# Optimization experiments

Measured on AMD Instinct MI355X. Metric: run time of the kernel, lower is better.

Reference implementation:

```python
import jax, jax.numpy as jnp
import numpy as np

N, F, H, K, T, O = 4096, 64, 64, 2, 5, 32  # nodes, in_feat, hidden, heads, temporal_steps, out


def setup_inputs() -> dict:
    key = jax.random.key(0)
    ks = jax.random.split(key, 12)
    s = 0.05
    return {
        "node_features": jax.random.normal(ks[0], (N, F), jnp.float32),
        "adj_matrix": jax.random.randint(ks[1], (N, N), 0, 2, jnp.int32),
        "temporal_features": jax.random.normal(ks[2], (N, T, H), jnp.float32),
        # GAT params (stacked over K heads). Linear W: Wh = h @ W.T, so W_gat[k] is [H, F].
        "W_gat": jax.random.normal(ks[3], (K, H, F), jnp.float32) * s,
        "a_src": jax.random.normal(ks[4], (K, H), jnp.float32) * s,  # first half of a (repeat -> column/neighbor index)
        "a_dst": jax.random.normal(ks[5], (K, H), jnp.float32) * s,  # second half of a (repeat_interleave -> row/self index)
        # LSTM (1 layer, input K*H, hidden H), PyTorch gate order i,f,g,o
        "W_ih": jax.random.normal(ks[6], (4 * H, K * H), jnp.float32) * s,
        "W_hh": jax.random.normal(ks[7], (4 * H, H), jnp.float32) * s,
        "b_ih": jax.random.normal(ks[8], (4 * H,), jnp.float32) * s,
        "b_hh": jax.random.normal(ks[9], (4 * H,), jnp.float32) * s,
        # fc
        "fc_W": jax.random.normal(ks[10], (O, H), jnp.float32) * s,
        "fc_b": jax.random.normal(ks[11], (O,), jnp.float32) * s,
    }


def reference(node_features, adj_matrix, temporal_features,
              W_gat, a_src, a_dst, W_ih, W_hh, b_ih, b_hh, fc_W, fc_b):
    # ---- GAT heads (vectorized over K) ----
    Wh = jnp.einsum("nf,khf->knh", node_features, W_gat)          # [K,N,H]
    # a([Wh_i, Wh_j]) == a_src.Wh_j + a_dst.Wh_i; e[p,q] = lrelu(dst[p] + src[q])
    s_src = jnp.einsum("knh,kh->kn", Wh, a_src)                    # column term
    s_dst = jnp.einsum("knh,kh->kn", Wh, a_dst)                    # row term
    e = jax.nn.leaky_relu(s_dst[:, :, None] + s_src[:, None, :], 0.2)  # [K,N,N]
    e = jnp.where(adj_matrix[None, :, :] > 0, e, jnp.float32(-1e9))
    att = jax.nn.softmax(e, axis=-1)                               # dropout = identity (eval)
    h_prime = jax.nn.elu(jnp.einsum("kpq,kqh->kph", att, Wh))      # [K,N,H]
    h = jnp.transpose(h_prime, (1, 0, 2)).reshape(N, K * H)        # concat heads [N, K*H]
    # ---- LSTM over seq of length 1 (h.unsqueeze(1)); h0 = c0 = 0 ----
    gates = h @ W_ih.T + b_ih + b_hh                               # h0 @ W_hh.T == 0
    i, f, g, o = jnp.split(gates, 4, axis=-1)
    c = jax.nn.sigmoid(i) * jnp.tanh(g)                            # f * c0 == 0
    h_t = jax.nn.sigmoid(o) * jnp.tanh(c)                          # [N,H]
    return h_t @ fc_W.T + fc_b                                     # [N,O]
```

## Files before the change

### kernel.cpp

```cpp
#include <hip/hip_runtime.h>


#define NN 4096

typedef __attribute__((ext_vector_type(8))) short bf16x8;
typedef __attribute__((ext_vector_type(4))) float f32x4;

__device__ inline unsigned short bf_rne(float f) {
    unsigned u = __float_as_uint(f);
    u += 0x7fffu + ((u >> 16) & 1u);
    return (unsigned short)(u >> 16);
}

__device__ inline unsigned cvt_pk_bf16(float lo, float hi) {
    unsigned r;
    asm("v_cvt_pk_bf16_f32 %0, %1, %2" : "=v"(r) : "v"(lo), "v"(hi));
    return r;
}

__device__ inline float sigf(float x) { return 1.f / (1.f + __expf(-x)); }

__device__ inline unsigned pack16(const int4 a, const int4 b,
                                  const int4 c, const int4 d) {
    unsigned m = 0;
    m |= (a.x > 0) ? 0x0001u : 0u; m |= (a.y > 0) ? 0x0002u : 0u;
    m |= (a.z > 0) ? 0x0004u : 0u; m |= (a.w > 0) ? 0x0008u : 0u;
    m |= (b.x > 0) ? 0x0010u : 0u; m |= (b.y > 0) ? 0x0020u : 0u;
    m |= (b.z > 0) ? 0x0040u : 0u; m |= (b.w > 0) ? 0x0080u : 0u;
    m |= (c.x > 0) ? 0x0100u : 0u; m |= (c.y > 0) ? 0x0200u : 0u;
    m |= (c.z > 0) ? 0x0400u : 0u; m |= (c.w > 0) ? 0x0800u : 0u;
    m |= (d.x > 0) ? 0x1000u : 0u; m |= (d.y > 0) ? 0x2000u : 0u;
    m |= (d.z > 0) ? 0x4000u : 0u; m |= (d.w > 0) ? 0x8000u : 0u;
    return m;
}

__global__ __launch_bounds__(256) void prep_small(
    const float* __restrict__ X, const float* __restrict__ Wg,
    const float* __restrict__ a_src, const float* __restrict__ a_dst,
    const float* __restrict__ W_ih, const float* __restrict__ b_ih,
    const float* __restrict__ b_hh, const float* __restrict__ fc_W,
    unsigned short* __restrict__ whB, float* __restrict__ e1s,
    float* __restrict__ e2s, float* __restrict__ e1d, float* __restrict__ e2d,
    unsigned short* __restrict__ Wpk, unsigned short* __restrict__ fcb,
    float* __restrict__ biasg)
{
    __shared__ float X_lds[64][64];
    __shared__ float Wh_lds[64][65];
    __shared__ float spart[64][4][2];
    const int t = threadIdx.x;
    const int bid = blockIdx.x;

    if (bid >= 64) {
        const int idx = (bid - 64) * 256 + t;
        if (idx < 24576) {
            const int j = idx & 7, lane = (idx >> 3) & 63;
            const int k0 = (idx >> 9) & 3, tt = idx >> 11;
            const int jj = tt * 16 + (lane & 15);
            const int m = k0 * 32 + (lane >> 4) * 8 + j;
            const int sr = (jj < 64) ? jj : 64 + jj;
            Wpk[idx] = bf_rne(W_ih[sr * 128 + m]);
        } else if (idx < 26624) {
            const int o = idx - 24576;
            const int j = o & 7, lane = (o >> 3) & 63;
            const int k0 = (o >> 9) & 1, tt = o >> 10;
            const int row = tt * 16 + (lane & 15);
            const int m = k0 * 32 + (lane >> 4) * 8 + j;
            fcb[o] = bf_rne(fc_W[row * 64 + m]);
        } else if (idx < 26816) {
            const int j = idx - 26624;
            const int sr = (j < 64) ? j : 64 + j;
            biasg[j] = b_ih[sr] + b_hh[sr];
        }
        return;
    }

    const int n0 = bid * 64;
#pragma unroll
    for (int i = 0; i < 16; ++i) {
        int idx = t + i * 256;
        X_lds[idx >> 6][idx & 63] = X[n0 * 64 + idx];
    }
    __syncthreads();
    const int h = t & 63, rg = t >> 6;
    for (int k = 0; k < 2; ++k) {
        float acc[16];
#pragma unroll
        for (int r = 0; r < 16; ++r) acc[r] = 0.f;
        for (int f0 = 0; f0 < 64; f0 += 4) {
            const float4 w4 = *(const float4*)&Wg[(k * 64 + h) * 64 + f0];
#pragma unroll
            for (int r = 0; r < 16; ++r) {
                const float4 x4 = *(const float4*)&X_lds[rg * 16 + r][f0];
                acc[r] += w4.x * x4.x + w4.y * x4.y + w4.z * x4.z + w4.w * x4.w;
            }
        }
        if (k) __syncthreads();
#pragma unroll
        for (int r = 0; r < 16; ++r) Wh_lds[rg * 16 + r][h] = acc[r];
        __syncthreads();
        {
            const int r = t & 63, qa = t >> 6;
            float ps = 0.f, pd = 0.f;
#pragma unroll
            for (int i = 0; i < 16; ++i) {
                const int hh = qa * 16 + i;
                const float v = Wh_lds[r][hh];
                ps += v * a_src[k * 64 + hh];
                pd += v * a_dst[k * 64 + hh];
            }
            spart[r][qa][0] = ps;
            spart[r][qa][1] = pd;
        }
        {
#pragma unroll
            for (int pid = t; pid < 512; pid += 256) {
                const int n = pid & 15, qg = (pid >> 4) & 3;
                const int qb_loc = (pid >> 6) & 1, f = pid >> 7;
                const int qb = (n0 >> 5) + qb_loc;
                unsigned pk[4];
#pragma unroll
                for (int i = 0; i < 4; ++i) {
                    const int r = qb_loc * 32 + qg * 8 + 2 * i;
                    unsigned lo = bf_rne(Wh_lds[r][f * 16 + n]);
                    unsigned hi = bf_rne(Wh_lds[r + 1][f * 16 + n]);
                    pk[i] = lo | (hi << 16);
                }
                uint4* dst = (uint4*)&whB[(((k * 4 + f) * 128 + qb) * 512) + (qg * 16 + n) * 8];
                *dst = make_uint4(pk[0], pk[1], pk[2], pk[3]);
            }
        }
        __syncthreads();
        if (t < 64) {
            float s0 = spart[t][0][0] + spart[t][1][0] + spart[t][2][0] + spart[t][3][0];
            float s1 = spart[t][0][1] + spart[t][1][1] + spart[t][2][1] + spart[t][3][1];
            e1s[k * NN + n0 + t] = __expf(s0);
            e2s[k * NN + n0 + t] = __expf(0.2f * s0);
            e1d[k * NN + n0 + t] = __expf(s1);
            e2d[k * NN + n0 + t] = __expf(0.2f * s1);
        }
    }
}

__global__ __launch_bounds__(1024) void gat_attn(
    const int* __restrict__ adj,
    const unsigned short* __restrict__ whB,
    const float* __restrict__ e1s, const float* __restrict__ e2s,
    const float* __restrict__ e1d, const float* __restrict__ e2d,
    const unsigned short* __restrict__ Wpk, const unsigned short* __restrict__ fcb,
    const float* __restrict__ biasg, const float* __restrict__ fc_b,
    float* __restrict__ out)
{
    __shared__ float S_all[16][2][16][64];
    __shared__ float z_all[16][2][16];
    __shared__ unsigned short msk_lds[2][16][66];
    unsigned short* h_lds = (unsigned short*)&S_all[0][0][0][0];
    float* gate_lds = (float*)((char*)&S_all[0][0][0][0] + 4608);

    const int tid = threadIdx.x;
    const int wave = tid >> 6, lane = tid & 63;
    const int rloc = lane & 15, qg = lane >> 4;
    const int p0 = blockIdx.x * 16;
    const int p = p0 + rloc;

    const int4* __restrict__ arow = (const int4*)(adj + (long)(p0 + wave) * NN);

    const float e1p0 = e1d[p], e2p0 = e2d[p];
    const float e1p1 = e1d[NN + p], e2p1 = e2d[NN + p];
    const unsigned short* __restrict__ whB_l = whB + lane * 8;

    f32x4 acc[2][4];
#pragma unroll
    for (int k = 0; k < 2; ++k)
#pragma unroll
        for (int f = 0; f < 4; ++f)
            acc[k][f] = (f32x4){0.f, 0.f, 0.f, 0.f};
    float z0 = 0.f, z1 = 0.f;

    {
        const int4 a0 = arow[lane * 4 + 0];
        const int4 a1 = arow[lane * 4 + 1];
        const int4 a2 = arow[lane * 4 + 2];
        const int4 a3 = arow[lane * 4 + 3];
        msk_lds[0][wave][lane] = (unsigned short)pack16(a0, a1, a2, a3);
    }
    __syncthreads();

#pragma unroll
    for (int c = 0; c < 4; ++c) {
        int4 n0v, n1v, n2v, n3v;
        if (c < 3) {
            const int base = (c + 1) * 256 + lane * 4;
            n0v = arow[base + 0];
            n1v = arow[base + 1];
            n2v = arow[base + 2];
            n3v = arow[base + 3];
        }
#pragma unroll
        for (int kk = 0; kk < 2; ++kk) {
            const int q0 = c * 1024 + wave * 64 + kk * 32 + qg * 8;
            const int qb = c * 32 + wave * 2 + kk;
            const unsigned mm = msk_lds[c & 1][rloc][wave * 4 + kk * 2 + (qg >> 1)];
            const unsigned byte8 = (mm >> ((qg & 1) * 8)) & 0xffu;
            const float4 qa0 = *(const float4*)(e1s + q0);
            const float4 qa1 = *(const float4*)(e1s + q0 + 4);
            const float4 qb0 = *(const float4*)(e2s + q0);
            const float4 qb1 = *(const float4*)(e2s + q0 + 4);
            const float4 qc0 = *(const float4*)(e1s + NN + q0);
            const float4 qc1 = *(const float4*)(e1s + NN + q0 + 4);
            const float4 qd0 = *(const float4*)(e2s + NN + q0);
            const float4 qd1 = *(const float4*)(e2s + NN + q0 + 4);
            const float q1v0[8] = {qa0.x, qa0.y, qa0.z, qa0.w, qa1.x, qa1.y, qa1.z, qa1.w};
            const float q2v0[8] = {qb0.x, qb0.y, qb0.z, qb0.w, qb1.x, qb1.y, qb1.z, qb1.w};
            const float q1v1[8] = {qc0.x, qc0.y, qc0.z, qc0.w, qc1.x, qc1.y, qc1.z, qc1.w};
            const float q2v1[8] = {qd0.x, qd0.y, qd0.z, qd0.w, qd1.x, qd1.y, qd1.z, qd1.w};
            float w0a[8], w1a[8];
#pragma unroll
            for (int j = 0; j < 8; ++j) {
                const bool on = (byte8 & (1u << j)) != 0u;
                const float pp0 = e1p0 * q1v0[j];
                float w0 = pp0 > 1.f ? pp0 : e2p0 * q2v0[j];
                w0 = on ? w0 : 0.f;
                z0 += w0;
                w0a[j] = w0;
                const float pp1 = e1p1 * q1v1[j];
                float w1 = pp1 > 1.f ? pp1 : e2p1 * q2v1[j];
                w1 = on ? w1 : 0.f;
                z1 += w1;
                w1a[j] = w1;
            }
            union { bf16x8 v; unsigned w[4]; } fa0, fa1;
#pragma unroll
            for (int i = 0; i < 4; ++i) {
                fa0.w[i] = cvt_pk_bf16(w0a[2 * i], w0a[2 * i + 1]);
                fa1.w[i] = cvt_pk_bf16(w1a[2 * i], w1a[2 * i + 1]);
            }
#pragma unroll
            for (int f = 0; f < 4; ++f) {
                const bf16x8 b0 = *(const bf16x8*)(whB_l + ((f * 128 + qb) << 9));
                acc[0][f] = __builtin_amdgcn_mfma_f32_16x16x32_bf16(fa0.v, b0, acc[0][f], 0, 0, 0);
                const bf16x8 b1 = *(const bf16x8*)(whB_l + (((4 + f) * 128 + qb) << 9));
                acc[1][f] = __builtin_amdgcn_mfma_f32_16x16x32_bf16(fa1.v, b1, acc[1][f], 0, 0, 0);
            }
        }
        if (c < 3) {
            msk_lds[(c + 1) & 1][wave][lane] =
                (unsigned short)pack16(n0v, n1v, n2v, n3v);
            __syncthreads();
        }
    }
    z0 += __shfl_xor(z0, 16); z0 += __shfl_xor(z0, 32);
    z1 += __shfl_xor(z1, 16); z1 += __shfl_xor(z1, 32);
    if (lane < 16) { z_all[wave][0][lane] = z0; z_all[wave][1][lane] = z1; }
#pragma unroll
    for (int k = 0; k < 2; ++k)
#pragma unroll
        for (int f = 0; f < 4; ++f)
#pragma unroll
            for (int j = 0; j < 4; ++j)
                S_all[wave][k][qg * 4 + j][f * 16 + rloc] = acc[k][f][j];
    __syncthreads();
    float vreg[2]; int vk[2], vr[2], vh[2];
#pragma unroll
    for (int i = 0; i < 2; ++i) {
        const int idx = tid + i * 1024;
        const int k = idx >> 10, rr = (idx >> 6) & 15, hh = idx & 63;
        float s = 0.f, z = 0.f;
#pragma unroll
        for (int w = 0; w < 16; ++w) {
            s += S_all[w][k][rr][hh];
            z += z_all[w][k][rr];
        }
        float v = s / z;
        vreg[i] = v > 0.f ? v : expm1f(v);
        vk[i] = k; vr[i] = rr; vh[i] = hh;
    }
    __syncthreads();
#pragma unroll
    for (int i = 0; i < 2; ++i)
        h_lds[vr[i] * 136 + vk[i] * 64 + vh[i]] = bf_rne(vreg[i]);
    __syncthreads();

    const int c2 = lane & 15, g4 = lane >> 4;
    if (wave < 12) {
        const int t = wave;
        f32x4 ga = (f32x4){0.f, 0.f, 0.f, 0.f};
#pragma unroll
        for (int k0 = 0; k0 < 4; ++k0) {
            const bf16x8 a = *(const bf16x8*)&h_lds[c2 * 136 + k0 * 32 + g4 * 8];
            const bf16x8 b = *(const bf16x8*)&Wpk[((t * 4 + k0) * 64 + lane) * 8];
            ga = __builtin_amdgcn_mfma_f32_16x16x32_bf16(a, b, ga, 0, 0, 0);
        }
        const float bb = biasg[t * 16 + c2];
#pragma unroll
        for (int j = 0; j < 4; ++j)
            gate_lds[(t >> 2) * 1088 + (g4 * 4 + j) * 68 + (t & 3) * 16 + c2] = ga[j] + bb;
    }
    __syncthreads();
    {
        const int n = tid >> 6, hh = tid & 63;
        const float iv = gate_lds[n * 68 + hh];
        const float gv = gate_lds[1088 + n * 68 + hh];
        const float ov = gate_lds[2176 + n * 68 + hh];
        const float cv = sigf(iv) * tanhf(gv);
        const float htv = sigf(ov) * tanhf(cv);
        __syncthreads();
        h_lds[n * 136 + hh] = bf_rne(htv);
    }
    __syncthreads();
    if (wave < 2) {
        const int t2 = wave;
        f32x4 fa = (f32x4){0.f, 0.f, 0.f, 0.f};
#pragma unroll
        for (int k0 = 0; k0 < 2; ++k0) {
            const bf16x8 a = *(const bf16x8*)&h_lds[c2 * 136 + k0 * 32 + g4 * 8];
            const bf16x8 b = *(const bf16x8*)&fcb[((t2 * 2 + k0) * 64 + lane) * 8];
            fa = __builtin_amdgcn_mfma_f32_16x16x32_bf16(a, b, fa, 0, 0, 0);
        }
        const float fb = fc_b[t2 * 16 + c2];
#pragma unroll
        for (int j = 0; j < 4; ++j)
            out[(p0 + g4 * 4 + j) * 32 + t2 * 16 + c2] = fa[j] + fb;
    }
}

extern "C" void kernel_launch(void* const* d_in, const int* in_sizes, int n_in,
                              void* d_out, int out_size, void* d_ws, size_t ws_size,
                              hipStream_t stream) {
    const float* X     = (const float*)d_in[0];
    const int*   adj   = (const int*)d_in[1];
    const float* Wg    = (const float*)d_in[3];
    const float* a_src = (const float*)d_in[4];
    const float* a_dst = (const float*)d_in[5];
    const float* W_ih  = (const float*)d_in[6];
    const float* b_ih  = (const float*)d_in[8];
    const float* b_hh  = (const float*)d_in[9];
    const float* fc_W  = (const float*)d_in[10];
    const float* fc_b  = (const float*)d_in[11];
    float* out = (float*)d_out;

    char* ws = (char*)d_ws;
    unsigned short* whB = (unsigned short*)ws;
    float* e1s = (float*)(ws + (1 << 20));
    float* e2s = (float*)(ws + (1 << 20) + (32 << 10));
    float* e1d = (float*)(ws + (1 << 20) + (64 << 10));
    float* e2d = (float*)(ws + (1 << 20) + (96 << 10));
    char* ws2 = ws + (1 << 20) + (128 << 10);
    unsigned short* Wpk = (unsigned short*)ws2;
    unsigned short* fcb = (unsigned short*)(ws2 + (48 << 10));
    float* biasg = (float*)(ws2 + (52 << 10));

    hipLaunchKernelGGL(prep_small, dim3(169), dim3(256), 0, stream,
                       X, Wg, a_src, a_dst, W_ih, b_ih, b_hh, fc_W,
                       whB, e1s, e2s, e1d, e2d, Wpk, fcb, biasg);
    hipLaunchKernelGGL(gat_attn, dim3(256), dim3(1024), 0, stream,
                       adj, whB, e1s, e2s, e1d, e2d, Wpk, fcb, biasg, fc_b, out);
}
```

Measured before the change: 58.38 us.

## Coalesce adjacency row loads and prefetch mask two chunks ahead

Adjacency rows were read with each lane loading four consecutive int4s. Now each load instruction has consecutive lanes reading consecutive int4s (stride 64 across the four loads), which coalesces the global reads. The nibble packing of the 0/1 mask and the bit extraction from shared memory are remapped to fit this interleaved layout. The prefetch depth grows from one chunk to two, with register double buffering. This hides more of the global load latency at the cost of extra registers and more complex bit shuffling.

```diff
diff --git a/kernel.cpp b/kernel.cpp
--- a/kernel.cpp
+++ b/kernel.cpp
@@ -20,17 +20,12 @@
 
 __device__ inline float sigf(float x) { return 1.f / (1.f + __expf(-x)); }
 
-__device__ inline unsigned pack16(const int4 a, const int4 b,
-                                  const int4 c, const int4 d) {
+__device__ inline unsigned nib4(const int4 a) {
     unsigned m = 0;
-    m |= (a.x > 0) ? 0x0001u : 0u; m |= (a.y > 0) ? 0x0002u : 0u;
-    m |= (a.z > 0) ? 0x0004u : 0u; m |= (a.w > 0) ? 0x0008u : 0u;
-    m |= (b.x > 0) ? 0x0010u : 0u; m |= (b.y > 0) ? 0x0020u : 0u;
-    m |= (b.z > 0) ? 0x0040u : 0u; m |= (b.w > 0) ? 0x0080u : 0u;
-    m |= (c.x > 0) ? 0x0100u : 0u; m |= (c.y > 0) ? 0x0200u : 0u;
-    m |= (c.z > 0) ? 0x0400u : 0u; m |= (c.w > 0) ? 0x0800u : 0u;
-    m |= (d.x > 0) ? 0x1000u : 0u; m |= (d.y > 0) ? 0x2000u : 0u;
-    m |= (d.z > 0) ? 0x4000u : 0u; m |= (d.w > 0) ? 0x8000u : 0u;
+    m |= (a.x > 0) ? 1u : 0u;
+    m |= (a.y > 0) ? 2u : 0u;
+    m |= (a.z > 0) ? 4u : 0u;
+    m |= (a.w > 0) ? 8u : 0u;
     return m;
 }
 
@@ -152,7 +147,7 @@
 {
     __shared__ float S_all[16][2][16][64];
     __shared__ float z_all[16][2][16];
-    __shared__ unsigned short msk_lds[2][16][66];
+    __shared__ unsigned msk32[2][16][37];
     unsigned short* h_lds = (unsigned short*)&S_all[0][0][0][0];
     float* gate_lds = (float*)((char*)&S_all[0][0][0][0] + 4608);
 
@@ -162,7 +157,7 @@
     const int p0 = blockIdx.x * 16;
     const int p = p0 + rloc;
 
-    const int4* __restrict__ arow = (const int4*)(adj + (long)(p0 + wave) * NN);
+    const int4* __restrict__ arow4 = (const int4*)(adj + (long)(p0 + wave) * NN);
 
     const float e1p0 = e1d[p], e2p0 = e2d[p];
     const float e1p1 = e1d[NN + p], e2p1 = e2d[NN + p];
@@ -176,31 +171,33 @@
             acc[k][f] = (f32x4){0.f, 0.f, 0.f, 0.f};
     float z0 = 0.f, z1 = 0.f;
 
+    int4 pre[2][4];
+#pragma unroll
+    for (int o = 0; o < 4; ++o) pre[0][o] = arow4[o * 64 + lane];
+#pragma unroll
+    for (int o = 0; o < 4; ++o) pre[1][o] = arow4[256 + o * 64 + lane];
     {
-        const int4 a0 = arow[lane * 4 + 0];
-        const int4 a1 = arow[lane * 4 + 1];
-        const int4 a2 = arow[lane * 4 + 2];
-        const int4 a3 = arow[lane * 4 + 3];
-        msk_lds[0][wave][lane] = (unsigned short)pack16(a0, a1, a2, a3);
+        const unsigned pk = nib4(pre[0][0]) | (nib4(pre[0][1]) << 4) |
+                            (nib4(pre[0][2]) << 8) | (nib4(pre[0][3]) << 12);
+        ((unsigned short*)&msk32[0][wave][0])[lane] = (unsigned short)pk;
     }
     __syncthreads();
 
 #pragma unroll
     for (int c = 0; c < 4; ++c) {
-        int4 n0v, n1v, n2v, n3v;
-        if (c < 3) {
-            const int base = (c + 1) * 256 + lane * 4;
-            n0v = arow[base + 0];
-            n1v = arow[base + 1];
-            n2v = arow[base + 2];
-            n3v = arow[base + 3];
+        if (c + 2 < 4) {
+#pragma unroll
+            for (int o = 0; o < 4; ++o)
+                pre[c & 1][o] = arow4[(c + 2) * 256 + o * 64 + lane];
         }
 #pragma unroll
         for (int kk = 0; kk < 2; ++kk) {
             const int q0 = c * 1024 + wave * 64 + kk * 32 + qg * 8;
             const int qb = c * 32 + wave * 2 + kk;
-            const unsigned mm = msk_lds[c & 1][rloc][wave * 4 + kk * 2 + (qg >> 1)];
-            const unsigned byte8 = (mm >> ((qg & 1) * 8)) & 0xffu;
+            const unsigned W = msk32[c & 1][rloc][(wave & 3) * 8 + kk * 4 + qg];
+            const unsigned osel = (wave >> 2) * 4;
+            const unsigned byte8 = ((W >> osel) & 0xFu) |
+                                   (((W >> (16 + osel)) & 0xFu) << 4);
             const float4 qa0 = *(const float4*)(e1s + q0);
             const float4 qa1 = *(const float4*)(e1s + q0 + 4);
             const float4 qb0 = *(const float4*)(e2s + q0);
@@ -243,8 +240,9 @@
             }
         }
         if (c < 3) {
-            msk_lds[(c + 1) & 1][wave][lane] =
-                (unsigned short)pack16(n0v, n1v, n2v, n3v);
+            const unsigned pk = nib4(pre[(c + 1) & 1][0]) | (nib4(pre[(c + 1) & 1][1]) << 4) |
+                                (nib4(pre[(c + 1) & 1][2]) << 8) | (nib4(pre[(c + 1) & 1][3]) << 12);
+            ((unsigned short*)&msk32[(c + 1) & 1][wave][0])[lane] = (unsigned short)pk;
             __syncthreads();
         }
     }
```

Result: slower. 60.09 us (+2.9%).

## Split prep kernel into 16-node blocks and use nontemporal loads for adjacency

Applied to the files above, without the earlier changes.

The prep kernel now handles 16 nodes per block instead of 64, giving 256 compute blocks instead of 64 so more CUs are busy. It also computes both heads in one pass and writes the bf16-packed Wh in smaller 32-bit stores. The attention kernel reads the adjacency matrix with nontemporal loads to avoid polluting the cache with streamed data. The trade-off is more redundant reads of the weights per block and narrower stores.

```diff
diff --git a/kernel.cpp b/kernel.cpp
--- a/kernel.cpp
+++ b/kernel.cpp
@@ -5,6 +5,7 @@
 
 typedef __attribute__((ext_vector_type(8))) short bf16x8;
 typedef __attribute__((ext_vector_type(4))) float f32x4;
+typedef __attribute__((ext_vector_type(4))) int i32x4;
 
 __device__ inline unsigned short bf_rne(float f) {
     unsigned u = __float_as_uint(f);
@@ -20,8 +21,8 @@
 
 __device__ inline float sigf(float x) { return 1.f / (1.f + __expf(-x)); }
 
-__device__ inline unsigned pack16(const int4 a, const int4 b,
-                                  const int4 c, const int4 d) {
+__device__ inline unsigned pack16(const i32x4 a, const i32x4 b,
+                                  const i32x4 c, const i32x4 d) {
     unsigned m = 0;
     m |= (a.x > 0) ? 0x0001u : 0u; m |= (a.y > 0) ? 0x0002u : 0u;
     m |= (a.z > 0) ? 0x0004u : 0u; m |= (a.w > 0) ? 0x0008u : 0u;
@@ -34,7 +35,7 @@
     return m;
 }
 
-__global__ __launch_bounds__(256) void prep_small(
+__global__ __launch_bounds__(256) void prep_parallel(
     const float* __restrict__ X, const float* __restrict__ Wg,
     const float* __restrict__ a_src, const float* __restrict__ a_dst,
     const float* __restrict__ W_ih, const float* __restrict__ b_ih,
@@ -44,14 +45,14 @@
     unsigned short* __restrict__ Wpk, unsigned short* __restrict__ fcb,
     float* __restrict__ biasg)
 {
-    __shared__ float X_lds[64][64];
-    __shared__ float Wh_lds[64][65];
-    __shared__ float spart[64][4][2];
+    __shared__ float X_lds[16][64];
+    __shared__ float Wh_lds[2][16][68];
+    __shared__ float spart[32][8][2];
     const int t = threadIdx.x;
     const int bid = blockIdx.x;
 
-    if (bid >= 64) {
-        const int idx = (bid - 64) * 256 + t;
+    if (bid >= 256) {
+        const int idx = (bid - 256) * 256 + t;
         if (idx < 24576) {
             const int j = idx & 7, lane = (idx >> 3) & 63;
             const int k0 = (idx >> 9) & 3, tt = idx >> 11;
@@ -74,70 +75,75 @@
         return;
     }
 
-    const int n0 = bid * 64;
-#pragma unroll
-    for (int i = 0; i < 16; ++i) {
-        int idx = t + i * 256;
-        X_lds[idx >> 6][idx & 63] = X[n0 * 64 + idx];
-    }
-    __syncthreads();
-    const int h = t & 63, rg = t >> 6;
-    for (int k = 0; k < 2; ++k) {
-        float acc[16];
-#pragma unroll
-        for (int r = 0; r < 16; ++r) acc[r] = 0.f;
-        for (int f0 = 0; f0 < 64; f0 += 4) {
-            const float4 w4 = *(const float4*)&Wg[(k * 64 + h) * 64 + f0];
-#pragma unroll
-            for (int r = 0; r < 16; ++r) {
-                const float4 x4 = *(const float4*)&X_lds[rg * 16 + r][f0];
-                acc[r] += w4.x * x4.x + w4.y * x4.y + w4.z * x4.z + w4.w * x4.w;
-            }
-        }
-        if (k) __syncthreads();
-#pragma unroll
-        for (int r = 0; r < 16; ++r) Wh_lds[rg * 16 + r][h] = acc[r];
-        __syncthreads();
-        {
-            const int r = t & 63, qa = t >> 6;
-            float ps = 0.f, pd = 0.f;
-#pragma unroll
-            for (int i = 0; i < 16; ++i) {
-                const int hh = qa * 16 + i;
-                const float v = Wh_lds[r][hh];
-                ps += v * a_src[k * 64 + hh];
-                pd += v * a_dst[k * 64 + hh];
-            }
-            spart[r][qa][0] = ps;
-            spart[r][qa][1] = pd;
-        }
-        {
-#pragma unroll
-            for (int pid = t; pid < 512; pid += 256) {
-                const int n = pid & 15, qg = (pid >> 4) & 3;
-                const int qb_loc = (pid >> 6) & 1, f = pid >> 7;
-                const int qb = (n0 >> 5) + qb_loc;
-                unsigned pk[4];
-#pragma unroll
-                for (int i = 0; i < 4; ++i) {
-                    const int r = qb_loc * 32 + qg * 8 + 2 * i;
-                    unsigned lo = bf_rne(Wh_lds[r][f * 16 + n]);
-                    unsigned hi = bf_rne(Wh_lds[r + 1][f * 16 + n]);
-                    pk[i] = lo | (hi << 16);
-                }
-                uint4* dst = (uint4*)&whB[(((k * 4 + f) * 128 + qb) * 512) + (qg * 16 + n) * 8];
-                *dst = make_uint4(pk[0], pk[1], pk[2], pk[3]);
-            }
-        }
-        __syncthreads();
-        if (t < 64) {
-            float s0 = spart[t][0][0] + spart[t][1][0] + spart[t][2][0] + spart[t][3][0];
-            float s1 = spart[t][0][1] + spart[t][1][1] + spart[t][2][1] + spart[t][3][1];
-            e1s[k * NN + n0 + t] = __expf(s0);
-            e2s[k * NN + n0 + t] = __expf(0.2f * s0);
-            e1d[k * NN + n0 + t] = __expf(s1);
-            e2d[k * NN + n0 + t] = __expf(0.2f * s1);
-        }
+    const int n0 = bid * 16;
+    {
+        const float4 x4 = *(const float4*)&X[(long)n0 * 64 + t * 4];
+        *(float4*)&X_lds[t >> 4][(t & 15) * 4] = x4;
+    }
+    __syncthreads();
+    const int h = t & 63, grp = t >> 6;
+    float acc0[4] = {0.f, 0.f, 0.f, 0.f};
+    float acc1[4] = {0.f, 0.f, 0.f, 0.f};
+#pragma unroll
+    for (int f0 = 0; f0 < 64; f0 += 4) {
+        const float4 wa = *(const float4*)&Wg[h * 64 + f0];
+        const float4 wb = *(const float4*)&Wg[(64 + h) * 64 + f0];
+#pragma unroll
+        for (int r = 0; r < 4; ++r) {
+            const float4 x4 = *(const float4*)&X_lds[grp * 4 + r][f0];
+            acc0[r] += wa.x * x4.x + wa.y * x4.y + wa.z * x4.z + wa.w * x4.w;
+            acc1[r] += wb.x * x4.x + wb.y * x4.y + wb.z * x4.z + wb.w * x4.w;
+        }
+    }
+#pragma unroll
+    for (int r = 0; r < 4; ++r) {
+        Wh_lds[0][grp * 4 + r][h] = acc0[r];
+        Wh_lds[1][grp * 4 + r][h] = acc1[r];
+    }
+    __syncthreads();
+    {
+        const int r2 = t & 31, qa = t >> 5;
+        const int k = r2 >> 4, nd = r2 & 15;
+        float ps = 0.f, pd = 0.f;
+#pragma unroll
+        for (int i = 0; i < 8; ++i) {
+            const int hh = qa * 8 + i;
+            const float v = Wh_lds[k][nd][hh];
+            ps += v * a_src[k * 64 + hh];
+            pd += v * a_dst[k * 64 + hh];
+        }
+        spart[r2][qa][0] = ps;
+        spart[r2][qa][1] = pd;
+    }
+    {
+        const int qb = n0 >> 5;
+        const int qgbase = (n0 & 31) >> 3;
+#pragma unroll
+        for (int it = 0; it < 4; ++it) {
+            const int pid = t + it * 256;
+            const int j2 = pid & 3, qgl = (pid >> 2) & 1;
+            const int n = (pid >> 3) & 15, f = (pid >> 7) & 3, k = pid >> 9;
+            const int i0 = qgl * 8 + j2 * 2;
+            const unsigned lo = bf_rne(Wh_lds[k][i0][f * 16 + n]);
+            const unsigned hi = bf_rne(Wh_lds[k][i0 + 1][f * 16 + n]);
+            unsigned* dst = (unsigned*)&whB[(((k * 4 + f) * 128 + qb) * 512)
+                                            + ((qgbase + qgl) * 16 + n) * 8 + j2 * 2];
+            *dst = lo | (hi << 16);
+        }
+    }
+    __syncthreads();
+    if (t < 32) {
+        const int k = t >> 4, nd = t & 15;
+        float s0 = 0.f, s1 = 0.f;
+#pragma unroll
+        for (int qa = 0; qa < 8; ++qa) {
+            s0 += spart[t][qa][0];
+            s1 += spart[t][qa][1];
+        }
+        e1s[k * NN + n0 + nd] = __expf(s0);
+        e2s[k * NN + n0 + nd] = __expf(0.2f * s0);
+        e1d[k * NN + n0 + nd] = __expf(s1);
+        e2d[k * NN + n0 + nd] = __expf(0.2f * s1);
     }
 }
 
@@ -162,7 +168,7 @@
     const int p0 = blockIdx.x * 16;
     const int p = p0 + rloc;
 
-    const int4* __restrict__ arow = (const int4*)(adj + (long)(p0 + wave) * NN);
+    const i32x4* __restrict__ arow = (const i32x4*)(adj + (long)(p0 + wave) * NN);
 
     const float e1p0 = e1d[p], e2p0 = e2d[p];
     const float e1p1 = e1d[NN + p], e2p1 = e2d[NN + p];
@@ -177,23 +183,23 @@
     float z0 = 0.f, z1 = 0.f;
 
     {
-        const int4 a0 = arow[lane * 4 + 0];
-        const int4 a1 = arow[lane * 4 + 1];
-        const int4 a2 = arow[lane * 4 + 2];
-        const int4 a3 = arow[lane * 4 + 3];
+        const i32x4 a0 = __builtin_nontemporal_load(&arow[lane * 4 + 0]);
+        const i32x4 a1 = __builtin_nontemporal_load(&arow[lane * 4 + 1]);
+        const i32x4 a2 = __builtin_nontemporal_load(&arow[lane * 4 + 2]);
+        const i32x4 a3 = __builtin_nontemporal_load(&arow[lane * 4 + 3]);
         msk_lds[0][wave][lane] = (unsigned short)pack16(a0, a1, a2, a3);
     }
     __syncthreads();
 
 #pragma unroll
     for (int c = 0; c < 4; ++c) {
-        int4 n0v, n1v, n2v, n3v;
+        i32x4 n0v, n1v, n2v, n3v;
         if (c < 3) {
             const int base = (c + 1) * 256 + lane * 4;
-            n0v = arow[base + 0];
-            n1v = arow[base + 1];
-            n2v = arow[base + 2];
-            n3v = arow[base + 3];
+            n0v = __builtin_nontemporal_load(&arow[base + 0]);
+            n1v = __builtin_nontemporal_load(&arow[base + 1]);
+            n2v = __builtin_nontemporal_load(&arow[base + 2]);
+            n3v = __builtin_nontemporal_load(&arow[base + 3]);
         }
 #pragma unroll
         for (int kk = 0; kk < 2; ++kk) {
@@ -349,7 +355,7 @@
     unsigned short* fcb = (unsigned short*)(ws2 + (48 << 10));
     float* biasg = (float*)(ws2 + (52 << 10));
 
-    hipLaunchKernelGGL(prep_small, dim3(169), dim3(256), 0, stream,
+    hipLaunchKernelGGL(prep_parallel, dim3(361), dim3(256), 0, stream,
                        X, Wg, a_src, a_dst, W_ih, b_ih, b_hh, fc_W,
                        whB, e1s, e2s, e1d, e2d, Wpk, fcb, biasg);
     hipLaunchKernelGGL(gat_attn, dim3(256), dim3(1024), 0, stream,
```

After: 54.65 us. -6.4%, faster.
